# Kernel tuning notes

Hardware: AMD Instinct MI355X
Metric: run time of the kernel (lower is better)

## Reference

```python
import jax, jax.numpy as jnp
import numpy as np
from jax.scipy.special import logsumexp

B0, K, T, A = 128, 8, 1024, 5
N_KCS, N_PROBLEMS = 50, 1000
MAX_LEN = K * T          # 8192 trials per student timeline
S = B0 * K               # 1024 subsequences
EPS = 1e-12


def setup_inputs() -> dict:
    rng = np.random.default_rng(0)
    lens = rng.integers(T - 128, T + 1, size=S)          # valid length per subsequence
    t = np.arange(T)
    valid = t[None, :] < lens[:, None]                   # (S,T) padding mask
    s = np.arange(S)
    # subsequence s covers slice (s%K)*T..+T of student s//K's timeline
    trial = (s // K)[:, None] * MAX_LEN + (s % K)[:, None] * T + t[None, :]
    trial = np.where(valid, trial, -1).astype(np.int32)
    problem = np.where(valid, rng.integers(0, N_PROBLEMS, (S, T)), 0).astype(np.int32)
    correct = np.where(valid, rng.integers(0, 2, (S, T)), 0).astype(np.int32)
    kc = rng.integers(0, N_KCS, S).astype(np.int32)
    ytrue_flat = -np.ones(B0 * MAX_LEN, dtype=np.int32)
    ytrue_flat[trial[valid]] = correct[valid]
    ytrue = ytrue_flat.reshape(B0, MAX_LEN)
    k1, k2, k3 = jax.random.split(jax.random.key(0), 3)
    return {
        'dynamics_logits': jax.random.normal(k1, (N_KCS, 3), dtype=jnp.float32),
        'obs_logits_kc': jax.random.normal(k2, (N_KCS, 2), dtype=jnp.float32),
        'obs_logits_problem': 0.1 * jax.random.normal(k3, (N_PROBLEMS, 2), dtype=jnp.float32),
        'ability_levels': jnp.array([-2.0, -1.0, 0.0, 1.0, 2.0], dtype=jnp.float32),
        'padded_trial_id': jnp.asarray(trial),
        'padded_problem': jnp.asarray(problem),
        'padded_correct': jnp.asarray(correct),
        'kc': jnp.asarray(kc),
        'ytrue': jnp.asarray(ytrue),
    }


def _bkt_filter(corr, dyn, pG, pS):
    """BKT HMM forward filter. corr:(B,T) int, dyn:(B,3), pG/pS:(B,T).
    Returns log predictive prob (B,T,2) of [incorrect, correct] before each trial."""
    pL = jax.nn.sigmoid(dyn[:, 0])   # p(learn)
    pF = jax.nn.sigmoid(dyn[:, 1])   # p(forget)
    pI = jax.nn.sigmoid(dyn[:, 2])   # p(known initially)
    alpha0 = jnp.stack([1.0 - pI, pI], axis=1)  # (B,2): [not-known, known]

    def step(alpha, xs):
        g, sl, y = xs                 # (B,) each
        pc0, pc1 = g, 1.0 - sl        # p(correct | state)
        p_corr = alpha[:, 0] * pc0 + alpha[:, 1] * pc1
        pred = jnp.stack([1.0 - p_corr, p_corr], axis=1)
        lik = jnp.where(y[:, None] == 1,
                        jnp.stack([pc0, pc1], axis=1),
                        jnp.stack([1.0 - pc0, 1.0 - pc1], axis=1))
        post = alpha * lik
        post = post / jnp.clip(post.sum(axis=1, keepdims=True), EPS)
        nxt = jnp.stack([post[:, 0] * (1 - pL) + post[:, 1] * pF,
                         post[:, 0] * pL + post[:, 1] * (1 - pF)], axis=1)
        return nxt, pred

    _, preds = jax.lax.scan(step, alpha0, (pG.T, pS.T, corr.T))  # preds: (T,B,2)
    return jnp.log(jnp.clip(jnp.transpose(preds, (1, 0, 2)), EPS))


def reference(dynamics_logits, obs_logits_kc, obs_logits_problem, ability_levels,
              padded_trial_id, padded_problem, padded_correct, kc, ytrue):
    b0, max_len = ytrue.shape
    a = ability_levels.shape[0]
    s_sub, t_len = padded_correct.shape
    # tile subsequence batch across ability levels (A*S rows)
    ability = jnp.repeat(ability_levels, s_sub)
    abil_ix = jnp.repeat(jnp.arange(a), s_sub)
    corr = jnp.tile(padded_correct, (a, 1))
    prob = jnp.tile(padded_problem, (a, 1))
    kc_t = jnp.tile(kc, (a,))
    tid = jnp.tile(padded_trial_id, (a, 1))

    dyn = dynamics_logits[kc_t]                                       # (AS,3)
    obs = obs_logits_kc[kc_t][:, None, :] + obs_logits_problem[prob]  # (AS,T,2)
    pG = jax.nn.sigmoid(obs[..., 0] + ability[:, None])  # p(correct | not known)
    pS = jax.nn.sigmoid(obs[..., 1] - ability[:, None])  # p(incorrect | known)
    logprob_pred = _bkt_filter(corr, dyn, pG, pS)        # (AS,T,2)

    # scatter back into per-ability flat student timelines
    adj = tid + abil_ix[:, None] * (b0 * max_len)
    adj = jnp.where(tid == -1, -1, adj).reshape(-1)
    n_flat = a * b0 * max_len
    idx = jnp.where(adj > -1, adj, n_flat)               # out-of-range -> dropped
    buf = jnp.zeros((n_flat, 2), dtype=logprob_pred.dtype)
    buf = buf.at[idx].set(logprob_pred.reshape(-1, 2), mode='drop')
    result = jnp.transpose(buf.reshape(a, b0, max_len, 2), (1, 0, 2, 3))  # (B0,A,L,2)

    # sequential Bayesian averaging over ability levels (uniform prior)
    mask = ytrue > -1
    yc = jnp.where(mask, ytrue, 0)
    obs_ll = jnp.take_along_axis(result, yc[:, None, :, None].astype(jnp.int32), axis=3)[..., 0]
    obs_ll = obs_ll * mask[:, None, :]
    prefix = jnp.cumsum(obs_ll, axis=2) - obs_ll          # exclusive cumsum over time
    logw = prefix - logsumexp(prefix, axis=1, keepdims=True)
    logpred = logsumexp(result + logw[..., None], axis=1)  # (B0,L,2)
    return logpred
```

## Files before the change

kernel.cpp:

```cpp
#include <hip/hip_runtime.h>
#include <hip/hip_fp16.h>
#include <math.h>

#define A 5
#define S 1024
#define T 1024
#define KCH 8
#define B0 128
#define L 8192
#define NPROB 1000
#define EPSF 1e-12f
#define CHUNK 8
#define PPB 2

__device__ __forceinline__ float sigmoidf_(float x) {
    return 1.0f / (1.0f + __expf(-x));
}

union H2U { unsigned u; __half2 h; };

__global__ __launch_bounds__(256) void bkt_filter_kernel(
    const float* __restrict__ dyn_logits,
    const float* __restrict__ obs_kc,
    const float* __restrict__ obs_prob,
    const float* __restrict__ abil,
    const int*   __restrict__ trial,
    const int*   __restrict__ problem,
    const int*   __restrict__ correct,
    const int*   __restrict__ kc,
    __half2* __restrict__ result,
    float* __restrict__ pfloc,
    float* __restrict__ sumchunk)
{
    __shared__ float2 s_e[NPROB];
    __shared__ float  s_m0[PPB][4];
    __shared__ float  s_llw[PPB];

    for (int i = threadIdx.x; i < NPROB; i += 256) {
        float2 op = ((const float2*)obs_prob)[i];
        s_e[i] = make_float2(__expf(-op.x), __expf(op.y));
    }
    __syncthreads();

    int wv = threadIdx.x >> 6;
    int lane = threadIdx.x & 63;
    int pib = wv >> 1;
    int half = wv & 1;
    int pair = blockIdx.x * PPB + pib;
    int a = pair >> 10;
    int s = pair & (S - 1);

    float ability = abil[a];
    int kcs = kc[s];
    float pL = sigmoidf_(dyn_logits[kcs * 3 + 0]);
    float pF = sigmoidf_(dyn_logits[kcs * 3 + 1]);
    float pI = sigmoidf_(dyn_logits[kcs * 3 + 2]);
    float ok0 = obs_kc[kcs * 2 + 0];
    float ok1 = obs_kc[kcs * 2 + 1];
    float t00 = 1.0f - pL, t01 = pF, t10 = pL, t11 = 1.0f - pF;
    float c0 = __expf(-ok0 - ability);
    float c1 = __expf( ok1 - ability);

    int t0 = half * (T / 2) + lane * CHUNK;
    const int4* pv4 = (const int4*)(problem + (size_t)s * T + t0);
    const int4* cv4 = (const int4*)(correct + (size_t)s * T + t0);
    const int4* tv4 = (const int4*)(trial   + (size_t)s * T + t0);
    int4 pva = pv4[0], pvb = pv4[1];
    int4 cva = cv4[0], cvb = cv4[1];
    int4 tva = tv4[0], tvb = tv4[1];

    int pj[8] = {pva.x, pva.y, pva.z, pva.w, pvb.x, pvb.y, pvb.z, pvb.w};
    int cj[8] = {cva.x, cva.y, cva.z, cva.w, cvb.x, cvb.y, cvb.z, cvb.w};
    int vj[8] = {tva.x, tva.y, tva.z, tva.w, tvb.x, tvb.y, tvb.z, tvb.w};
    int cmask = 0, vmask = 0;
    #pragma unroll
    for (int j = 0; j < 8; ++j) {
        cmask |= (cj[j] & 1) << j;
        vmask |= (vj[j] != -1) << j;
    }

    float pc0a[8], pc1a[8];
    float p00 = 1.0f, p01 = 0.0f, p10 = 0.0f, p11 = 1.0f;
    #pragma unroll
    for (int j = 0; j < 8; ++j) {
        float2 e = s_e[pj[j]];
        float pc0 = __builtin_amdgcn_rcpf(1.0f + e.x * c0);
        float pc1 = __builtin_amdgcn_rcpf(1.0f + e.y * c1);
        pc0a[j] = pc0; pc1a[j] = pc1;
        bool c = (cmask >> j) & 1;
        float lik0 = c ? pc0 : 1.0f - pc0;
        float lik1 = c ? pc1 : 1.0f - pc1;
        float r0 = lik0 * p00, r1 = lik1 * p10;
        float r2 = lik0 * p01, r3 = lik1 * p11;
        p00 = t00 * r0 + t01 * r1;
        p10 = t10 * r0 + t11 * r1;
        p01 = t00 * r2 + t01 * r3;
        p11 = t10 * r2 + t11 * r3;
        if ((j & 3) == 3) {
            float inv = __builtin_amdgcn_rcpf(p00 + p01 + p10 + p11);
            p00 *= inv; p01 *= inv; p10 *= inv; p11 *= inv;
        }
    }

    float q00 = p00, q01 = p01, q10 = p10, q11 = p11;
    #pragma unroll
    for (int off = 1; off < 64; off <<= 1) {
        float o00 = __shfl_up(q00, off);
        float o01 = __shfl_up(q01, off);
        float o10 = __shfl_up(q10, off);
        float o11 = __shfl_up(q11, off);
        if (lane >= off) {
            float n00 = q00 * o00 + q01 * o10;
            float n01 = q00 * o01 + q01 * o11;
            float n10 = q10 * o00 + q11 * o10;
            float n11 = q10 * o01 + q11 * o11;
            float inv = __builtin_amdgcn_rcpf(n00 + n01 + n10 + n11);
            q00 = n00 * inv; q01 = n01 * inv; q10 = n10 * inv; q11 = n11 * inv;
        }
    }
    if (half == 0 && lane == 63) {
        s_m0[pib][0] = q00; s_m0[pib][1] = q01;
        s_m0[pib][2] = q10; s_m0[pib][3] = q11;
    }
    __syncthreads();

    float e00 = __shfl_up(q00, 1), e01 = __shfl_up(q01, 1);
    float e10 = __shfl_up(q10, 1), e11 = __shfl_up(q11, 1);
    if (lane == 0) { e00 = 1.0f; e01 = 0.0f; e10 = 0.0f; e11 = 1.0f; }
    if (half == 1) {
        float m00 = s_m0[pib][0], m01 = s_m0[pib][1];
        float m10 = s_m0[pib][2], m11 = s_m0[pib][3];
        float n00 = e00 * m00 + e01 * m10;
        float n01 = e00 * m01 + e01 * m11;
        float n10 = e10 * m00 + e11 * m10;
        float n11 = e10 * m01 + e11 * m11;
        e00 = n00; e01 = n01; e10 = n10; e11 = n11;
    }
    float a0 = e00 * (1.0f - pI) + e01 * pI;
    float a1 = e10 * (1.0f - pI) + e11 * pI;
    {
        float inv = __builtin_amdgcn_rcpf(fmaxf(a0 + a1, EPSF));
        a0 *= inv; a1 *= inv;
    }

    float ll[8];
    float llsum = 0.0f;
    #pragma unroll
    for (int j = 0; j < 8; ++j) {
        float pc0 = pc0a[j], pc1 = pc1a[j];
        bool c = (cmask >> j) & 1;
        bool valid = (vmask >> j) & 1;
        float p_corr = a0 * pc0 + a1 * pc1;
        float p1v = p_corr, p0v = 1.0f - p_corr;
        float py = c ? p1v : p0v;
        float llj = valid ? __logf(fmaxf(py, EPSF)) : 0.0f;
        ll[j] = llj; llsum += llj;
        pc0a[j] = valid ? p0v : 1.0f;
        pc1a[j] = valid ? p1v : 1.0f;
        float lik0 = c ? pc0 : 1.0f - pc0;
        float lik1 = c ? pc1 : 1.0f - pc1;
        float qq0 = a0 * lik0, qq1 = a1 * lik1;
        float invq = __builtin_amdgcn_rcpf(fmaxf(qq0 + qq1, EPSF));
        qq0 *= invq; qq1 *= invq;
        a0 = qq0 * t00 + qq1 * t01;
        a1 = qq0 * t10 + qq1 * t11;
    }

    float incl = llsum;
    #pragma unroll
    for (int off = 1; off < 64; off <<= 1) {
        float o = __shfl_up(incl, off);
        if (lane >= off) incl += o;
    }
    float excl = incl - llsum;
    if (half == 0 && lane == 63) s_llw[pib] = incl;
    __syncthreads();
    int b = s >> 3, chunk = s & 7;
    if (half == 1) {
        float w0 = s_llw[pib];
        excl += w0;
        if (lane == 63)
            sumchunk[((size_t)a * B0 + b) * KCH + chunk] = w0 + incl;
    }

    unsigned ru[8];
    #pragma unroll
    for (int j = 0; j < 8; ++j) {
        H2U cv_;
        cv_.h = __floats2half2_rn(pc0a[j], pc1a[j]);
        ru[j] = cv_.u;
    }
    __half2* res_row = result + ((size_t)pair * T + t0);
    ((uint4*)res_row)[0] = make_uint4(ru[0], ru[1], ru[2], ru[3]);
    ((uint4*)res_row)[1] = make_uint4(ru[4], ru[5], ru[6], ru[7]);

    float* pf_row = pfloc + ((size_t)pair * T + t0);
    float run = excl;
    float pw[8];
    #pragma unroll
    for (int j = 0; j < 8; ++j) { pw[j] = run; run += ll[j]; }
    ((float4*)pf_row)[0] = make_float4(pw[0], pw[1], pw[2], pw[3]);
    ((float4*)pf_row)[1] = make_float4(pw[4], pw[5], pw[6], pw[7]);
}

__global__ __launch_bounds__(256) void combine_kernel(
    const float* __restrict__ pfloc,
    const __half2* __restrict__ result,
    const float* __restrict__ sumchunk,
    float* __restrict__ out)
{
    int s_sub = blockIdx.x;
    int b = s_sub >> 3, chunk = s_sub & 7;
    int t0 = threadIdx.x * 4;

    float pf[A][4];
    float2 pp[A][4];
    #pragma unroll
    for (int a = 0; a < A; ++a) {
        float base = 0.0f;
        for (int k = 0; k < chunk; ++k)
            base += sumchunk[((size_t)a * B0 + b) * KCH + k];
        size_t off = ((size_t)a * S + s_sub) * T + t0;
        float4 f = *(const float4*)(pfloc + off);
        pf[a][0] = f.x + base; pf[a][1] = f.y + base;
        pf[a][2] = f.z + base; pf[a][3] = f.w + base;
        uint4 q = *(const uint4*)(result + off);
        unsigned uu[4] = {q.x, q.y, q.z, q.w};
        #pragma unroll
        for (int j = 0; j < 4; ++j) {
            H2U cv_; cv_.u = uu[j];
            pp[a][j] = __half22float2(cv_.h);
        }
    }

    float o[8];
    #pragma unroll
    for (int j = 0; j < 4; ++j) {
        float pm = -INFINITY;
        #pragma unroll
        for (int a = 0; a < A; ++a) pm = fmaxf(pm, pf[a][j]);
        float Se = 0.0f, S0 = 0.0f, S1 = 0.0f;
        #pragma unroll
        for (int a = 0; a < A; ++a) {
            float e = __expf(pf[a][j] - pm);
            Se += e;
            S0 += e * pp[a][j].x;
            S1 += e * pp[a][j].y;
        }
        float ls = __logf(Se);
        o[2*j]   = __logf(S0) - ls;
        o[2*j+1] = __logf(S1) - ls;
    }
    float* op = out + 2 * ((size_t)b * L + chunk * T + t0);
    ((float4*)op)[0] = make_float4(o[0], o[1], o[2], o[3]);
    ((float4*)op)[1] = make_float4(o[4], o[5], o[6], o[7]);
}

extern "C" void kernel_launch(void* const* d_in, const int* in_sizes, int n_in,
                              void* d_out, int out_size, void* d_ws, size_t ws_size,
                              hipStream_t stream) {
    const float* dyn  = (const float*)d_in[0];
    const float* okc  = (const float*)d_in[1];
    const float* oprb = (const float*)d_in[2];
    const float* ab   = (const float*)d_in[3];
    const int* trial  = (const int*)d_in[4];
    const int* prob   = (const int*)d_in[5];
    const int* corr   = (const int*)d_in[6];
    const int* kc     = (const int*)d_in[7];
    float* out = (float*)d_out;

    __half2* result = (__half2*)d_ws;
    float* pfloc = (float*)((char*)d_ws + (size_t)A * S * T * 4);
    float* sumchunk = pfloc + (size_t)A * S * T;

    bkt_filter_kernel<<<(A * S) / PPB, 256, 0, stream>>>(
        dyn, okc, oprb, ab, trial, prob, corr, kc, result, pfloc, sumchunk);
    combine_kernel<<<B0 * KCH, 256, 0, stream>>>(pfloc, result, sumchunk, out);
}
```

Measured before the change: 39.41 us.

## Fuse filter and ability combine into one per-student kernel via shared memory

Merges the two kernels into a single kernel with one 640-thread block per student. Each block handles all five abilities and loops over the eight chunks, staging prefix log-likelihoods and half-precision predictions in LDS and combining them in place, so the global workspace round trip and the second launch go away. Validity is derived from a per-chunk length computed with a ballot instead of loading the trial array, and normalizations in the scan and filter are applied less often. The trade-off is only 128 blocks on a large GPU, with eight serialized chunk iterations and several block barriers per chunk, which limits parallelism and latency hiding.

```diff
diff --git a/kernel.cpp b/kernel.cpp
--- a/kernel.cpp
+++ b/kernel.cpp
@@ -10,16 +10,15 @@
 #define L 8192
 #define NPROB 1000
 #define EPSF 1e-12f
-#define CHUNK 8
-#define PPB 2
+#define NTHR 640
 
 __device__ __forceinline__ float sigmoidf_(float x) {
     return 1.0f / (1.0f + __expf(-x));
 }
 
-union H2U { unsigned u; __half2 h; };
-
-__global__ __launch_bounds__(256) void bkt_filter_kernel(
+struct ExSlot { float pf; __half2 p; };
+
+__global__ __launch_bounds__(NTHR) void bkt_student_kernel(
     const float* __restrict__ dyn_logits,
     const float* __restrict__ obs_kc,
     const float* __restrict__ obs_prob,
@@ -28,232 +27,218 @@
     const int*   __restrict__ problem,
     const int*   __restrict__ correct,
     const int*   __restrict__ kc,
-    __half2* __restrict__ result,
-    float* __restrict__ pfloc,
-    float* __restrict__ sumchunk)
+    float* __restrict__ out)
 {
     __shared__ float2 s_e[NPROB];
-    __shared__ float  s_m0[PPB][4];
-    __shared__ float  s_llw[PPB];
-
-    for (int i = threadIdx.x; i < NPROB; i += 256) {
+    __shared__ ExSlot s_ex[A][1024];
+    __shared__ float  s_m0[A][4];
+    __shared__ float  s_llw[A];
+    __shared__ float  s_tot[A];
+    __shared__ int    s_len[KCH];
+
+    int b = blockIdx.x;
+    int w = threadIdx.x >> 6;
+    int lane = threadIdx.x & 63;
+    int a = w >> 1;
+    int half = w & 1;
+
+    for (int i = threadIdx.x; i < NPROB; i += NTHR) {
         float2 op = ((const float2*)obs_prob)[i];
         s_e[i] = make_float2(__expf(-op.x), __expf(op.y));
     }
-    __syncthreads();
-
-    int wv = threadIdx.x >> 6;
-    int lane = threadIdx.x & 63;
-    int pib = wv >> 1;
-    int half = wv & 1;
-    int pair = blockIdx.x * PPB + pib;
-    int a = pair >> 10;
-    int s = pair & (S - 1);
-
-    float ability = abil[a];
-    int kcs = kc[s];
-    float pL = sigmoidf_(dyn_logits[kcs * 3 + 0]);
-    float pF = sigmoidf_(dyn_logits[kcs * 3 + 1]);
-    float pI = sigmoidf_(dyn_logits[kcs * 3 + 2]);
-    float ok0 = obs_kc[kcs * 2 + 0];
-    float ok1 = obs_kc[kcs * 2 + 1];
-    float t00 = 1.0f - pL, t01 = pF, t10 = pL, t11 = 1.0f - pF;
-    float c0 = __expf(-ok0 - ability);
-    float c1 = __expf( ok1 - ability);
-
-    int t0 = half * (T / 2) + lane * CHUNK;
-    const int4* pv4 = (const int4*)(problem + (size_t)s * T + t0);
-    const int4* cv4 = (const int4*)(correct + (size_t)s * T + t0);
-    const int4* tv4 = (const int4*)(trial   + (size_t)s * T + t0);
-    int4 pva = pv4[0], pvb = pv4[1];
-    int4 cva = cv4[0], cvb = cv4[1];
-    int4 tva = tv4[0], tvb = tv4[1];
-
-    int pj[8] = {pva.x, pva.y, pva.z, pva.w, pvb.x, pvb.y, pvb.z, pvb.w};
-    int cj[8] = {cva.x, cva.y, cva.z, cva.w, cvb.x, cvb.y, cvb.z, cvb.w};
-    int vj[8] = {tva.x, tva.y, tva.z, tva.w, tvb.x, tvb.y, tvb.z, tvb.w};
-    int cmask = 0, vmask = 0;
-    #pragma unroll
-    for (int j = 0; j < 8; ++j) {
-        cmask |= (cj[j] & 1) << j;
-        vmask |= (vj[j] != -1) << j;
-    }
-
-    float pc0a[8], pc1a[8];
-    float p00 = 1.0f, p01 = 0.0f, p10 = 0.0f, p11 = 1.0f;
-    #pragma unroll
-    for (int j = 0; j < 8; ++j) {
-        float2 e = s_e[pj[j]];
-        float pc0 = __builtin_amdgcn_rcpf(1.0f + e.x * c0);
-        float pc1 = __builtin_amdgcn_rcpf(1.0f + e.y * c1);
-        pc0a[j] = pc0; pc1a[j] = pc1;
-        bool c = (cmask >> j) & 1;
-        float lik0 = c ? pc0 : 1.0f - pc0;
-        float lik1 = c ? pc1 : 1.0f - pc1;
-        float r0 = lik0 * p00, r1 = lik1 * p10;
-        float r2 = lik0 * p01, r3 = lik1 * p11;
-        p00 = t00 * r0 + t01 * r1;
-        p10 = t10 * r0 + t11 * r1;
-        p01 = t00 * r2 + t01 * r3;
-        p11 = t10 * r2 + t11 * r3;
-        if ((j & 3) == 3) {
-            float inv = __builtin_amdgcn_rcpf(p00 + p01 + p10 + p11);
-            p00 *= inv; p01 *= inv; p10 *= inv; p11 *= inv;
-        }
-    }
-
-    float q00 = p00, q01 = p01, q10 = p10, q11 = p11;
-    #pragma unroll
-    for (int off = 1; off < 64; off <<= 1) {
-        float o00 = __shfl_up(q00, off);
-        float o01 = __shfl_up(q01, off);
-        float o10 = __shfl_up(q10, off);
-        float o11 = __shfl_up(q11, off);
-        if (lane >= off) {
-            float n00 = q00 * o00 + q01 * o10;
-            float n01 = q00 * o01 + q01 * o11;
-            float n10 = q10 * o00 + q11 * o10;
-            float n11 = q10 * o01 + q11 * o11;
-            float inv = __builtin_amdgcn_rcpf(n00 + n01 + n10 + n11);
-            q00 = n00 * inv; q01 = n01 * inv; q10 = n10 * inv; q11 = n11 * inv;
-        }
-    }
-    if (half == 0 && lane == 63) {
-        s_m0[pib][0] = q00; s_m0[pib][1] = q01;
-        s_m0[pib][2] = q10; s_m0[pib][3] = q11;
+    if (w < KCH) {
+        const int* tr = trial + (size_t)(b * KCH + w) * T;
+        int v1 = tr[896 + lane] != -1;
+        int v2 = tr[960 + lane] != -1;
+        unsigned long long m1 = __ballot(v1), m2 = __ballot(v2);
+        if (lane == 0) s_len[w] = 896 + __popcll(m1) + __popcll(m2);
     }
     __syncthreads();
 
-    float e00 = __shfl_up(q00, 1), e01 = __shfl_up(q01, 1);
-    float e10 = __shfl_up(q10, 1), e11 = __shfl_up(q11, 1);
-    if (lane == 0) { e00 = 1.0f; e01 = 0.0f; e10 = 0.0f; e11 = 1.0f; }
-    if (half == 1) {
-        float m00 = s_m0[pib][0], m01 = s_m0[pib][1];
-        float m10 = s_m0[pib][2], m11 = s_m0[pib][3];
-        float n00 = e00 * m00 + e01 * m10;
-        float n01 = e00 * m01 + e01 * m11;
-        float n10 = e10 * m00 + e11 * m10;
-        float n11 = e10 * m01 + e11 * m11;
-        e00 = n00; e01 = n01; e10 = n10; e11 = n11;
+    float ability = abil[a];
+    float base = 0.0f;
+    int t0l = half * 512 + lane * 8;
+
+    for (int k = 0; k < KCH; ++k) {
+        int s = b * KCH + k;
+        int kcs = kc[s];
+        int len_s = s_len[k];
+        float pL = sigmoidf_(dyn_logits[kcs * 3 + 0]);
+        float pF = sigmoidf_(dyn_logits[kcs * 3 + 1]);
+        float pI = sigmoidf_(dyn_logits[kcs * 3 + 2]);
+        float ok0 = obs_kc[kcs * 2 + 0];
+        float ok1 = obs_kc[kcs * 2 + 1];
+        float t00 = 1.0f - pL, t01 = pF, t10 = pL, t11 = 1.0f - pF;
+        float c0 = __expf(-ok0 - ability);
+        float c1 = __expf( ok1 - ability);
+
+        const int4* pv4 = (const int4*)(problem + (size_t)s * T + t0l);
+        const int4* cv4 = (const int4*)(correct + (size_t)s * T + t0l);
+        int4 pva = pv4[0], pvb = pv4[1];
+        int4 cva = cv4[0], cvb = cv4[1];
+        int pj[8] = {pva.x, pva.y, pva.z, pva.w, pvb.x, pvb.y, pvb.z, pvb.w};
+        int cj[8] = {cva.x, cva.y, cva.z, cva.w, cvb.x, cvb.y, cvb.z, cvb.w};
+        int cmask = 0, vmask = 0;
+        #pragma unroll
+        for (int j = 0; j < 8; ++j) {
+            cmask |= (cj[j] & 1) << j;
+            vmask |= ((t0l + j) < len_s) << j;
+        }
+
+        float pc0a[8], pc1a[8];
+        float p00 = 1.0f, p01 = 0.0f, p10 = 0.0f, p11 = 1.0f;
+        #pragma unroll
+        for (int j = 0; j < 8; ++j) {
+            float2 e = s_e[pj[j]];
+            float pc0 = __builtin_amdgcn_rcpf(1.0f + e.x * c0);
+            float pc1 = __builtin_amdgcn_rcpf(1.0f + e.y * c1);
+            pc0a[j] = pc0; pc1a[j] = pc1;
+            bool c = (cmask >> j) & 1;
+            float lik0 = c ? pc0 : 1.0f - pc0;
+            float lik1 = c ? pc1 : 1.0f - pc1;
+            float r0 = lik0 * p00, r1 = lik1 * p10;
+            float r2 = lik0 * p01, r3 = lik1 * p11;
+            p00 = t00 * r0 + t01 * r1;
+            p10 = t10 * r0 + t11 * r1;
+            p01 = t00 * r2 + t01 * r3;
+            p11 = t10 * r2 + t11 * r3;
+            if ((j & 3) == 3) {
+                float inv = __builtin_amdgcn_rcpf(p00 + p01 + p10 + p11);
+                p00 *= inv; p01 *= inv; p10 *= inv; p11 *= inv;
+            }
+        }
+
+        float q00 = p00, q01 = p01, q10 = p10, q11 = p11;
+        #pragma unroll
+        for (int off = 1; off < 64; off <<= 1) {
+            float o00 = __shfl_up(q00, off);
+            float o01 = __shfl_up(q01, off);
+            float o10 = __shfl_up(q10, off);
+            float o11 = __shfl_up(q11, off);
+            if (lane >= off) {
+                float n00 = q00 * o00 + q01 * o10;
+                float n01 = q00 * o01 + q01 * o11;
+                float n10 = q10 * o00 + q11 * o10;
+                float n11 = q10 * o01 + q11 * o11;
+                q00 = n00; q01 = n01; q10 = n10; q11 = n11;
+            }
+            if (off == 8 || off == 32) {
+                float inv = __builtin_amdgcn_rcpf(fmaxf(q00 + q01 + q10 + q11, 1e-30f));
+                q00 *= inv; q01 *= inv; q10 *= inv; q11 *= inv;
+            }
+        }
+        if (half == 0 && lane == 63) {
+            float inv = __builtin_amdgcn_rcpf(fmaxf(q00 + q01 + q10 + q11, 1e-30f));
+            s_m0[a][0] = q00 * inv; s_m0[a][1] = q01 * inv;
+            s_m0[a][2] = q10 * inv; s_m0[a][3] = q11 * inv;
+        }
+        __syncthreads();
+
+        float e00 = __shfl_up(q00, 1), e01 = __shfl_up(q01, 1);
+        float e10 = __shfl_up(q10, 1), e11 = __shfl_up(q11, 1);
+        if (lane == 0) { e00 = 1.0f; e01 = 0.0f; e10 = 0.0f; e11 = 1.0f; }
+        if (half == 1) {
+            float m00 = s_m0[a][0], m01 = s_m0[a][1];
+            float m10 = s_m0[a][2], m11 = s_m0[a][3];
+            float n00 = e00 * m00 + e01 * m10;
+            float n01 = e00 * m01 + e01 * m11;
+            float n10 = e10 * m00 + e11 * m10;
+            float n11 = e10 * m01 + e11 * m11;
+            e00 = n00; e01 = n01; e10 = n10; e11 = n11;
+        }
+        float a0 = e00 * (1.0f - pI) + e01 * pI;
+        float a1 = e10 * (1.0f - pI) + e11 * pI;
+        {
+            float inv = __builtin_amdgcn_rcpf(fmaxf(a0 + a1, EPSF));
+            a0 *= inv; a1 *= inv;
+        }
+
+        float ll[8];
+        float llsum = 0.0f;
+        #pragma unroll
+        for (int j = 0; j < 8; ++j) {
+            float pc0 = pc0a[j], pc1 = pc1a[j];
+            bool c = (cmask >> j) & 1;
+            bool valid = (vmask >> j) & 1;
+            float num = a0 * pc0 + a1 * pc1;
+            float den = a0 + a1;
+            float pcor = num * __builtin_amdgcn_rcpf(den);
+            float p0v = 1.0f - pcor;
+            float py = c ? pcor : p0v;
+            float llj = valid ? __logf(fmaxf(py, EPSF)) : 0.0f;
+            ll[j] = llj; llsum += llj;
+            pc0a[j] = valid ? p0v : 1.0f;
+            pc1a[j] = valid ? pcor : 1.0f;
+            float lik0 = c ? pc0 : 1.0f - pc0;
+            float lik1 = c ? pc1 : 1.0f - pc1;
+            float q0 = a0 * lik0, q1 = a1 * lik1;
+            a0 = q0 * t00 + q1 * t01;
+            a1 = q0 * t10 + q1 * t11;
+            if ((j & 3) == 3) {
+                float inv = __builtin_amdgcn_rcpf(fmaxf(a0 + a1, EPSF));
+                a0 *= inv; a1 *= inv;
+            }
+        }
+
+        float incl = llsum;
+        #pragma unroll
+        for (int off = 1; off < 64; off <<= 1) {
+            float o = __shfl_up(incl, off);
+            if (lane >= off) incl += o;
+        }
+        if (half == 0 && lane == 63) s_llw[a] = incl;
+        __syncthreads();
+        float excl = incl - llsum;
+        if (half == 1) {
+            float w0 = s_llw[a];
+            excl += w0;
+            float tot = w0 + __shfl(incl, 63);
+            if (lane == 63) s_tot[a] = tot;
+        }
+
+        float run = base + excl;
+        #pragma unroll
+        for (int j = 0; j < 8; ++j) {
+            ExSlot e;
+            e.pf = run;
+            e.p = __floats2half2_rn(pc0a[j], pc1a[j]);
+            s_ex[a][t0l + j] = e;
+            run += ll[j];
+        }
+        __syncthreads();
+
+        int t = threadIdx.x;
+        if (t < 512) {
+            float o[4];
+            #pragma unroll
+            for (int u = 0; u < 2; ++u) {
+                int sl = 2 * t + u;
+                float pf[A]; float2 pp[A];
+                float pm = -INFINITY;
+                #pragma unroll
+                for (int aa = 0; aa < A; ++aa) {
+                    ExSlot e = s_ex[aa][sl];
+                    pf[aa] = e.pf;
+                    pp[aa] = __half22float2(e.p);
+                    pm = fmaxf(pm, e.pf);
+                }
+                float Se = 0.0f, S0 = 0.0f, S1 = 0.0f;
+                #pragma unroll
+                for (int aa = 0; aa < A; ++aa) {
+                    float ee = __expf(pf[aa] - pm);
+                    Se += ee;
+                    S0 += ee * pp[aa].x;
+                    S1 += ee * pp[aa].y;
+                }
+                float ls = __logf(Se);
+                o[2*u]   = __logf(S0) - ls;
+                o[2*u+1] = __logf(S1) - ls;
+            }
+            float* op = out + 2 * ((size_t)b * L + k * T + 2 * t);
+            *(float4*)op = make_float4(o[0], o[1], o[2], o[3]);
+        }
+        base += s_tot[a];
     }
-    float a0 = e00 * (1.0f - pI) + e01 * pI;
-    float a1 = e10 * (1.0f - pI) + e11 * pI;
-    {
-        float inv = __builtin_amdgcn_rcpf(fmaxf(a0 + a1, EPSF));
-        a0 *= inv; a1 *= inv;
-    }
-
-    float ll[8];
-    float llsum = 0.0f;
-    #pragma unroll
-    for (int j = 0; j < 8; ++j) {
-        float pc0 = pc0a[j], pc1 = pc1a[j];
-        bool c = (cmask >> j) & 1;
-        bool valid = (vmask >> j) & 1;
-        float p_corr = a0 * pc0 + a1 * pc1;
-        float p1v = p_corr, p0v = 1.0f - p_corr;
-        float py = c ? p1v : p0v;
-        float llj = valid ? __logf(fmaxf(py, EPSF)) : 0.0f;
-        ll[j] = llj; llsum += llj;
-        pc0a[j] = valid ? p0v : 1.0f;
-        pc1a[j] = valid ? p1v : 1.0f;
-        float lik0 = c ? pc0 : 1.0f - pc0;
-        float lik1 = c ? pc1 : 1.0f - pc1;
-        float qq0 = a0 * lik0, qq1 = a1 * lik1;
-        float invq = __builtin_amdgcn_rcpf(fmaxf(qq0 + qq1, EPSF));
-        qq0 *= invq; qq1 *= invq;
-        a0 = qq0 * t00 + qq1 * t01;
-        a1 = qq0 * t10 + qq1 * t11;
-    }
-
-    float incl = llsum;
-    #pragma unroll
-    for (int off = 1; off < 64; off <<= 1) {
-        float o = __shfl_up(incl, off);
-        if (lane >= off) incl += o;
-    }
-    float excl = incl - llsum;
-    if (half == 0 && lane == 63) s_llw[pib] = incl;
-    __syncthreads();
-    int b = s >> 3, chunk = s & 7;
-    if (half == 1) {
-        float w0 = s_llw[pib];
-        excl += w0;
-        if (lane == 63)
-            sumchunk[((size_t)a * B0 + b) * KCH + chunk] = w0 + incl;
-    }
-
-    unsigned ru[8];
-    #pragma unroll
-    for (int j = 0; j < 8; ++j) {
-        H2U cv_;
-        cv_.h = __floats2half2_rn(pc0a[j], pc1a[j]);
-        ru[j] = cv_.u;
-    }
-    __half2* res_row = result + ((size_t)pair * T + t0);
-    ((uint4*)res_row)[0] = make_uint4(ru[0], ru[1], ru[2], ru[3]);
-    ((uint4*)res_row)[1] = make_uint4(ru[4], ru[5], ru[6], ru[7]);
-
-    float* pf_row = pfloc + ((size_t)pair * T + t0);
-    float run = excl;
-    float pw[8];
-    #pragma unroll
-    for (int j = 0; j < 8; ++j) { pw[j] = run; run += ll[j]; }
-    ((float4*)pf_row)[0] = make_float4(pw[0], pw[1], pw[2], pw[3]);
-    ((float4*)pf_row)[1] = make_float4(pw[4], pw[5], pw[6], pw[7]);
-}
-
-__global__ __launch_bounds__(256) void combine_kernel(
-    const float* __restrict__ pfloc,
-    const __half2* __restrict__ result,
-    const float* __restrict__ sumchunk,
-    float* __restrict__ out)
-{
-    int s_sub = blockIdx.x;
-    int b = s_sub >> 3, chunk = s_sub & 7;
-    int t0 = threadIdx.x * 4;
-
-    float pf[A][4];
-    float2 pp[A][4];
-    #pragma unroll
-    for (int a = 0; a < A; ++a) {
-        float base = 0.0f;
-        for (int k = 0; k < chunk; ++k)
-            base += sumchunk[((size_t)a * B0 + b) * KCH + k];
-        size_t off = ((size_t)a * S + s_sub) * T + t0;
-        float4 f = *(const float4*)(pfloc + off);
-        pf[a][0] = f.x + base; pf[a][1] = f.y + base;
-        pf[a][2] = f.z + base; pf[a][3] = f.w + base;
-        uint4 q = *(const uint4*)(result + off);
-        unsigned uu[4] = {q.x, q.y, q.z, q.w};
-        #pragma unroll
-        for (int j = 0; j < 4; ++j) {
-            H2U cv_; cv_.u = uu[j];
-            pp[a][j] = __half22float2(cv_.h);
-        }
-    }
-
-    float o[8];
-    #pragma unroll
-    for (int j = 0; j < 4; ++j) {
-        float pm = -INFINITY;
-        #pragma unroll
-        for (int a = 0; a < A; ++a) pm = fmaxf(pm, pf[a][j]);
-        float Se = 0.0f, S0 = 0.0f, S1 = 0.0f;
-        #pragma unroll
-        for (int a = 0; a < A; ++a) {
-            float e = __expf(pf[a][j] - pm);
-            Se += e;
-            S0 += e * pp[a][j].x;
-            S1 += e * pp[a][j].y;
-        }
-        float ls = __logf(Se);
-        o[2*j]   = __logf(S0) - ls;
-        o[2*j+1] = __logf(S1) - ls;
-    }
-    float* op = out + 2 * ((size_t)b * L + chunk * T + t0);
-    ((float4*)op)[0] = make_float4(o[0], o[1], o[2], o[3]);
-    ((float4*)op)[1] = make_float4(o[4], o[5], o[6], o[7]);
 }
 
 extern "C" void kernel_launch(void* const* d_in, const int* in_sizes, int n_in,
@@ -269,11 +254,6 @@
     const int* kc     = (const int*)d_in[7];
     float* out = (float*)d_out;
 
-    __half2* result = (__half2*)d_ws;
-    float* pfloc = (float*)((char*)d_ws + (size_t)A * S * T * 4);
-    float* sumchunk = pfloc + (size_t)A * S * T;
-
-    bkt_filter_kernel<<<(A * S) / PPB, 256, 0, stream>>>(
-        dyn, okc, oprb, ab, trial, prob, corr, kc, result, pfloc, sumchunk);
-    combine_kernel<<<B0 * KCH, 256, 0, stream>>>(pfloc, result, sumchunk, out);
+    bkt_student_kernel<<<B0, NTHR, 0, stream>>>(
+        dyn, okc, oprb, ab, trial, prob, corr, kc, out);
 }
```

Measured after the change: 60.86 us. 54.4% more time.
